# Performance work log

Measured on AMD Instinct MI355X. Metric: run time of the kernel, lower is better.

Reference implementation:

```python
import jax, jax.numpy as jnp
import numpy as np

T = 1.0  # temperature from __init__ (t=1)


def setup_inputs() -> dict:
    key = jax.random.key(0)
    k1, k2, k3 = jax.random.split(key, 3)
    N, C, D = 262144, 1024, 128
    feats = jax.random.normal(k1, (N, D), dtype=jnp.float32)
    prototypes = jax.random.normal(k2, (C, D), dtype=jnp.float32)
    labels = jax.random.randint(k3, (N,), 0, C, dtype=jnp.int64)
    return {"feats": feats, "prototypes": prototypes, "labels": labels}


def _dce_loss(feats, prototypes, labels):
    # same math as sqrt(sum((x[:,None,:]-y)**2, -1)) without the NxCxD tensor.
    x_sq = jnp.sum(feats * feats, axis=-1, keepdims=True)          # [N,1]
    y_sq = jnp.sum(prototypes * prototypes, axis=-1)               # [C]
    xy = jnp.einsum('nd,cd->nc', feats, prototypes)                # [N,C]
    sq_dist = jnp.maximum(x_sq + y_sq[None, :] - 2.0 * xy, 0.0)
    logits = -jnp.sqrt(sq_dist) / T                                # [N,C]
    logp = jax.nn.log_softmax(logits, axis=-1)
    nll = -jnp.take_along_axis(logp, labels[:, None], axis=-1)[:, 0]
    return jnp.mean(nll)  # CrossEntropyLoss default reduction='mean'


def reference(feats, prototypes, labels):
    return _dce_loss(feats, prototypes, labels)
```

## Files before the change

### kernel.cpp

```cpp
#include <hip/hip_runtime.h>
#include <hip/hip_bf16.h>

typedef __bf16 bf16x8 __attribute__((ext_vector_type(8)));
typedef __bf16 bf16x2 __attribute__((ext_vector_type(2)));
typedef float f32x4 __attribute__((ext_vector_type(4)));

#define LN2f 0.6931471805599453f
#define CEf  2.0402785445f

__global__ void dce_prep(const float* __restrict__ protos,
                         unsigned short* __restrict__ bpf,
                         float* __restrict__ ysqn) {
    int c = blockIdx.x;
    int lane = threadIdx.x;
    float2 f = ((const float2*)(protos))[c * 64 + lane];
    int d0 = lane * 2;
    int kk = d0 >> 5, sub = d0 & 31, lg = sub >> 3, e = sub & 7;
    size_t o = (((size_t)((c >> 4) * 4 + kk) * 64) + lg * 16 + (c & 15)) * 8 + e;
    bf16x2 h;
    h.x = (__bf16)f.x;
    h.y = (__bf16)f.y;
    *(bf16x2*)(bpf + o) = h;
    float xs = f.x * f.x + f.y * f.y;
#pragma unroll
    for (int d = 1; d < 64; d <<= 1) xs += __shfl_xor(xs, d);
    if (lane == 0) ysqn[c] = -0.5f * xs;
}

__global__ __launch_bounds__(256, 4) void dce_main(
    const float* __restrict__ feats,
    const float* __restrict__ protos,
    const unsigned short* __restrict__ bpf,
    const float* __restrict__ ysqn,
    const int* __restrict__ labels,
    float* __restrict__ partials, int C) {
    const int tid = threadIdx.x;
    const int lane = tid & 63;
    const int w = tid >> 6;
    const int row0 = blockIdx.x * 128;
    const int rbase = row0 + w * 32;
    const int lr = lane & 15;
    const int lg = lane >> 4;

    const int r1 = row0 + (tid >> 1);
    const int half = tid & 1;
    const int lab = labels[r1];
    const float4* fx = (const float4*)feats + (size_t)r1 * 32 + half * 16;
    const float4* px = (const float4*)protos + (size_t)lab * 32 + half * 16;
    float xx = 0.f, yy = 0.f, xy = 0.f;
#pragma unroll
    for (int i = 0; i < 16; ++i) {
        float4 f = fx[i], p = px[i];
        xx = fmaf(f.x, f.x, fmaf(f.y, f.y, fmaf(f.z, f.z, fmaf(f.w, f.w, xx))));
        yy = fmaf(p.x, p.x, fmaf(p.y, p.y, fmaf(p.z, p.z, fmaf(p.w, p.w, yy))));
        xy = fmaf(f.x, p.x, fmaf(f.y, p.y, fmaf(f.z, p.z, fmaf(f.w, p.w, xy))));
    }
    xx += __shfl_xor(xx, 1);
    yy += __shfl_xor(yy, 1);
    xy += __shfl_xor(xy, 1);
    const float ld = __builtin_amdgcn_sqrtf(fmaxf(fmaf(-2.f, xy, xx + yy), 0.f));

    bf16x8 a[2][4];
    const float4* f4 = (const float4*)feats;
#pragma unroll
    for (int m = 0; m < 2; ++m) {
        size_t r = (size_t)(rbase + m * 16 + lr);
#pragma unroll
        for (int kk = 0; kk < 4; ++kk) {
            size_t idx = r * 32 + kk * 8 + lg * 2;
            float4 lo = f4[idx];
            float4 hi = f4[idx + 1];
            bf16x8 v;
            v[0] = (__bf16)lo.x; v[1] = (__bf16)lo.y; v[2] = (__bf16)lo.z; v[3] = (__bf16)lo.w;
            v[4] = (__bf16)hi.x; v[5] = (__bf16)hi.y; v[6] = (__bf16)hi.z; v[7] = (__bf16)hi.w;
            a[m][kk] = v;
        }
    }

    float pre[2][4];
#pragma unroll
    for (int m = 0; m < 2; ++m)
#pragma unroll
        for (int reg = 0; reg < 4; ++reg)
            pre[m][reg] = -0.5f * __shfl(xx, 2 * (m * 16 + lg * 4 + reg));

    float lacc[2][4];
#pragma unroll
    for (int m = 0; m < 2; ++m)
#pragma unroll
        for (int reg = 0; reg < 4; ++reg) lacc[m][reg] = 0.f;

    const char* bp = (const char*)bpf + (size_t)lane * 16;
    const float* ysp = ysqn + lr;

    const int t0 = ((w << 4) + ((blockIdx.x & 15) << 2)) & 63;

#define LOADB(dst, yq, t)                                                     \
    {                                                                         \
        const int tt_ = (t0 + (t)) & 63;                                      \
        _Pragma("unroll") for (int kk = 0; kk < 4; ++kk)                      \
            dst[kk] = *(const bf16x8*)(bp + (size_t)tt_ * 4096 + kk * 1024);  \
        yq = ysp[tt_ * 16];                                                   \
    }

#define COMPUTE(b, yq)                                                          \
    {                                                                           \
        _Pragma("unroll") for (int m = 0; m < 2; ++m) {                         \
            f32x4 acc;                                                          \
            acc[0] = pre[m][0] + yq;                                            \
            acc[1] = pre[m][1] + yq;                                            \
            acc[2] = pre[m][2] + yq;                                            \
            acc[3] = pre[m][3] + yq;                                            \
            acc = __builtin_amdgcn_mfma_f32_16x16x32_bf16(a[m][0], b[0], acc, 0, 0, 0); \
            acc = __builtin_amdgcn_mfma_f32_16x16x32_bf16(a[m][1], b[1], acc, 0, 0, 0); \
            acc = __builtin_amdgcn_mfma_f32_16x16x32_bf16(a[m][2], b[2], acc, 0, 0, 0); \
            acc = __builtin_amdgcn_mfma_f32_16x16x32_bf16(a[m][3], b[3], acc, 0, 0, 0); \
            _Pragma("unroll") for (int reg = 0; reg < 4; ++reg) {               \
                float s = __builtin_amdgcn_sqrtf(-acc[reg]);   \
                lacc[m][reg] += __builtin_amdgcn_exp2f(s * -CEf);               \
            }                                                                   \
        }                                                                       \
    }

    bf16x8 bA[4], bB[4];
    float yqA, yqB;
    LOADB(bA, yqA, 0);
    const int nt = C >> 4;
    for (int t = 0; t < nt - 2; t += 2) {
        LOADB(bB, yqB, t + 1);
        COMPUTE(bA, yqA);
        LOADB(bA, yqA, t + 2);
        COMPUTE(bB, yqB);
    }
    LOADB(bB, yqB, nt - 1);
    COMPUTE(bA, yqA);
    COMPUTE(bB, yqB);

#undef LOADB
#undef COMPUTE

    float ssum = 0.f;
#pragma unroll
    for (int m = 0; m < 2; ++m)
#pragma unroll
        for (int reg = 0; reg < 4; ++reg) {
            float l = lacc[m][reg];
            l += __shfl_xor(l, 1);
            l += __shfl_xor(l, 2);
            l += __shfl_xor(l, 4);
            l += __shfl_xor(l, 8);
            float ldv = __shfl(ld, 2 * (m * 16 + lg * 4 + reg));
            if (lr == 0) ssum += ldv + LN2f * __builtin_amdgcn_logf(l);
        }
    ssum += __shfl_xor(ssum, 16);
    ssum += __shfl_xor(ssum, 32);

    __shared__ float red[4];
    if (lane == 0) red[w] = ssum;
    __syncthreads();
    if (tid == 0) partials[blockIdx.x] = red[0] + red[1] + red[2] + red[3];
}

__global__ void dce_finish(const float* __restrict__ partials,
                           float* __restrict__ out, int nblocks, float invN) {
    int tid = threadIdx.x;
    float s = 0.f;
    for (int i = tid; i < nblocks; i += 256) s += partials[i];
#pragma unroll
    for (int d = 1; d < 64; d <<= 1) s += __shfl_xor(s, d);
    __shared__ float red[4];
    if ((tid & 63) == 0) red[tid >> 6] = s;
    __syncthreads();
    if (tid == 0) out[0] = (red[0] + red[1] + red[2] + red[3]) * invN;
}

extern "C" void kernel_launch(void* const* d_in, const int* in_sizes, int n_in,
                              void* d_out, int out_size, void* d_ws, size_t ws_size,
                              hipStream_t stream) {
    const float* feats = (const float*)d_in[0];
    const float* protos = (const float*)d_in[1];
    const int* labels = (const int*)d_in[2];
    const int N = in_sizes[2];
    const int C = in_sizes[1] / 128;
    float* out = (float*)d_out;

    unsigned short* bpf = (unsigned short*)d_ws;
    float* ysqn = (float*)((char*)d_ws + (size_t)C * 128 * 2);
    float* partials = ysqn + C;
    const int nblocks = N / 128;

    dce_prep<<<C, 64, 0, stream>>>(protos, bpf, ysqn);
    dce_main<<<nblocks, 256, 0, stream>>>(feats, protos, bpf, ysqn, labels, partials, C);
    dce_finish<<<1, 256, 0, stream>>>(partials, out, nblocks, 1.0f / (float)N);
}
```

Measured before the change: 138.8 us.

## Replace exp2 with bit-trick exponential, halve block size, use nontemporal feature loads

Replaces the hardware exp2 in the inner softmax loop with a Schraudolph-style exponential: a single fma whose result is converted to int and reinterpreted as float. This removes one transcendental per logit. Blocks shrink from 256 to 128 threads with twice as many blocks, the prototype tile start offset per wave is adjusted, and feature loads for the MFMA operands use nontemporal hints. The approximate exponential adds a few percent relative error per term, which may shift the loss value.

```diff
diff --git a/kernel.cpp b/kernel.cpp
--- a/kernel.cpp
+++ b/kernel.cpp
@@ -7,6 +7,8 @@
 
 #define LN2f 0.6931471805599453f
 #define CEf  2.0402785445f
+#define EXPA (-CEf * 8388608.0f)
+#define EXPB ((127.0f - 0.0437f) * 8388608.0f)
 
 __global__ void dce_prep(const float* __restrict__ protos,
                          unsigned short* __restrict__ bpf,
@@ -27,7 +29,7 @@
     if (lane == 0) ysqn[c] = -0.5f * xs;
 }
 
-__global__ __launch_bounds__(256, 4) void dce_main(
+__global__ __launch_bounds__(128, 4) void dce_main(
     const float* __restrict__ feats,
     const float* __restrict__ protos,
     const unsigned short* __restrict__ bpf,
@@ -37,7 +39,7 @@
     const int tid = threadIdx.x;
     const int lane = tid & 63;
     const int w = tid >> 6;
-    const int row0 = blockIdx.x * 128;
+    const int row0 = blockIdx.x * 64;
     const int rbase = row0 + w * 32;
     const int lr = lane & 15;
     const int lg = lane >> 4;
@@ -45,15 +47,16 @@
     const int r1 = row0 + (tid >> 1);
     const int half = tid & 1;
     const int lab = labels[r1];
-    const float4* fx = (const float4*)feats + (size_t)r1 * 32 + half * 16;
-    const float4* px = (const float4*)protos + (size_t)lab * 32 + half * 16;
+    const f32x4* fx = (const f32x4*)(feats) + (size_t)r1 * 32 + half * 16;
+    const f32x4* px = (const f32x4*)(protos) + (size_t)lab * 32 + half * 16;
     float xx = 0.f, yy = 0.f, xy = 0.f;
 #pragma unroll
     for (int i = 0; i < 16; ++i) {
-        float4 f = fx[i], p = px[i];
-        xx = fmaf(f.x, f.x, fmaf(f.y, f.y, fmaf(f.z, f.z, fmaf(f.w, f.w, xx))));
-        yy = fmaf(p.x, p.x, fmaf(p.y, p.y, fmaf(p.z, p.z, fmaf(p.w, p.w, yy))));
-        xy = fmaf(f.x, p.x, fmaf(f.y, p.y, fmaf(f.z, p.z, fmaf(f.w, p.w, xy))));
+        f32x4 f = fx[i];
+        f32x4 p = px[i];
+        xx = fmaf(f[0], f[0], fmaf(f[1], f[1], fmaf(f[2], f[2], fmaf(f[3], f[3], xx))));
+        yy = fmaf(p[0], p[0], fmaf(p[1], p[1], fmaf(p[2], p[2], fmaf(p[3], p[3], yy))));
+        xy = fmaf(f[0], p[0], fmaf(f[1], p[1], fmaf(f[2], p[2], fmaf(f[3], p[3], xy))));
     }
     xx += __shfl_xor(xx, 1);
     yy += __shfl_xor(yy, 1);
@@ -61,18 +64,18 @@
     const float ld = __builtin_amdgcn_sqrtf(fmaxf(fmaf(-2.f, xy, xx + yy), 0.f));
 
     bf16x8 a[2][4];
-    const float4* f4 = (const float4*)feats;
+    const f32x4* f4 = (const f32x4*)feats;
 #pragma unroll
     for (int m = 0; m < 2; ++m) {
         size_t r = (size_t)(rbase + m * 16 + lr);
 #pragma unroll
         for (int kk = 0; kk < 4; ++kk) {
             size_t idx = r * 32 + kk * 8 + lg * 2;
-            float4 lo = f4[idx];
-            float4 hi = f4[idx + 1];
+            f32x4 lo = __builtin_nontemporal_load(f4 + idx);
+            f32x4 hi = __builtin_nontemporal_load(f4 + idx + 1);
             bf16x8 v;
-            v[0] = (__bf16)lo.x; v[1] = (__bf16)lo.y; v[2] = (__bf16)lo.z; v[3] = (__bf16)lo.w;
-            v[4] = (__bf16)hi.x; v[5] = (__bf16)hi.y; v[6] = (__bf16)hi.z; v[7] = (__bf16)hi.w;
+            v[0] = (__bf16)lo[0]; v[1] = (__bf16)lo[1]; v[2] = (__bf16)lo[2]; v[3] = (__bf16)lo[3];
+            v[4] = (__bf16)hi[0]; v[5] = (__bf16)hi[1]; v[6] = (__bf16)hi[2]; v[7] = (__bf16)hi[3];
             a[m][kk] = v;
         }
     }
@@ -93,7 +96,7 @@
     const char* bp = (const char*)bpf + (size_t)lane * 16;
     const float* ysp = ysqn + lr;
 
-    const int t0 = ((w << 4) + ((blockIdx.x & 15) << 2)) & 63;
+    const int t0 = (((blockIdx.x & 15) << 2) + (w << 5)) & 63;
 
 #define LOADB(dst, yq, t)                                                     \
     {                                                                         \
@@ -116,8 +119,9 @@
             acc = __builtin_amdgcn_mfma_f32_16x16x32_bf16(a[m][2], b[2], acc, 0, 0, 0); \
             acc = __builtin_amdgcn_mfma_f32_16x16x32_bf16(a[m][3], b[3], acc, 0, 0, 0); \
             _Pragma("unroll") for (int reg = 0; reg < 4; ++reg) {               \
-                float s = __builtin_amdgcn_sqrtf(-acc[reg]);   \
-                lacc[m][reg] += __builtin_amdgcn_exp2f(s * -CEf);               \
+                float s_ = __builtin_amdgcn_sqrtf(-acc[reg]);  \
+                int i_ = (int)fmaf(s_, EXPA, EXPB);            \
+                lacc[m][reg] += __int_as_float(i_);                             \
             }                                                                   \
         }                                                                       \
     }
@@ -155,10 +159,10 @@
     ssum += __shfl_xor(ssum, 16);
     ssum += __shfl_xor(ssum, 32);
 
-    __shared__ float red[4];
+    __shared__ float red[2];
     if (lane == 0) red[w] = ssum;
     __syncthreads();
-    if (tid == 0) partials[blockIdx.x] = red[0] + red[1] + red[2] + red[3];
+    if (tid == 0) partials[blockIdx.x] = red[0] + red[1];
 }
 
 __global__ void dce_finish(const float* __restrict__ partials,
@@ -187,9 +191,9 @@
     unsigned short* bpf = (unsigned short*)d_ws;
     float* ysqn = (float*)((char*)d_ws + (size_t)C * 128 * 2);
     float* partials = ysqn + C;
-    const int nblocks = N / 128;
+    const int nblocks = N / 64;
 
     dce_prep<<<C, 64, 0, stream>>>(protos, bpf, ysqn);
-    dce_main<<<nblocks, 256, 0, stream>>>(feats, protos, bpf, ysqn, labels, partials, C);
+    dce_main<<<nblocks, 128, 0, stream>>>(feats, protos, bpf, ysqn, labels, partials, C);
     dce_finish<<<1, 256, 0, stream>>>(partials, out, nblocks, 1.0f / (float)N);
 }
```

Measured after the change: 140.9 us. About the same (+1.6%).
